# Kernel optimization log

Measured on AMD Instinct MI355X. Metric: run time of the kernel, lower is better.

## Reference

```python
import jax, jax.numpy as jnp
import numpy as np
import math

DIMS = [2048, 1024, 512, 4096]
NH, DK, DV = 16, 64, 64
BS = 8192
D_MODEL = NH * DK  # 1024


def setup_inputs() -> dict:
    key = jax.random.key(0)
    ks = jax.random.split(key, 3 * len(DIMS) + 5)
    inp = {"input_data": jax.random.normal(ks[0], (BS, sum(DIMS)), jnp.float32)}
    ki = 1
    for i, d in enumerate(DIMS):
        inp[f"wq{i}"] = jax.random.normal(ks[ki], (NH * DK, d), jnp.float32) * 0.02; ki += 1
        inp[f"wk{i}"] = jax.random.normal(ks[ki], (NH * DK, d), jnp.float32) * 0.02; ki += 1
        inp[f"wv{i}"] = jax.random.normal(ks[ki], (NH * DV, d), jnp.float32) * 0.02; ki += 1
    inp["fc_w"] = jax.random.normal(ks[ki], (NH * DV, NH * DV), jnp.float32) * 0.02; ki += 1
    inp["fc_b"] = jax.random.normal(ks[ki], (NH * DV,), jnp.float32) * 0.02; ki += 1
    inp["ln_g"] = jnp.ones((NH * DV,), jnp.float32)
    inp["ln_b"] = jnp.zeros((NH * DV,), jnp.float32)
    return inp


def _forward(input_data, wqs, wks, wvs, fc_w, fc_b, ln_g, ln_b):
    bs = input_data.shape[0]
    M = len(DIMS)
    offs = np.cumsum([0] + DIMS)
    # per-modality projections; stack into [bs, M, NH*D]
    xs = [input_data[:, offs[i]:offs[i + 1]] for i in range(M)]
    q = jnp.stack([x @ w.T for x, w in zip(xs, wqs)], axis=1)  # [bs, M, NH*DK]
    k = jnp.stack([x @ w.T for x, w in zip(xs, wks)], axis=1)
    v = jnp.stack([x @ w.T for x, w in zip(xs, wvs)], axis=1)  # [bs, M, NH*DV]
    residual = v  # v.transpose(1,2).view == original stacked v
    qh = q.reshape(bs, M, NH, DK).transpose(0, 2, 1, 3)  # [bs, NH, M, DK]
    kh = k.reshape(bs, M, NH, DK).transpose(0, 2, 1, 3)
    vh = v.reshape(bs, M, NH, DV).transpose(0, 2, 1, 3)
    scores = jnp.einsum('bhqd,bhkd->bhqk', qh, kh) / math.sqrt(DK)
    attn = jax.nn.softmax(scores, axis=-1)  # [bs, NH, M, M]
    ctx = jnp.einsum('bhqk,bhkd->bhqd', attn, vh)  # [bs, NH, M, DV]
    ctx = ctx.transpose(0, 2, 1, 3).reshape(bs, M, NH * DV)
    out = ctx @ fc_w.T + fc_b  # dropout is identity (p=0 / eval)
    out = out + residual
    mu = jnp.mean(out, axis=-1, keepdims=True)
    var = jnp.var(out, axis=-1, keepdims=True)
    out = (out - mu) / jnp.sqrt(var + 1e-6) * ln_g + ln_b
    return out, attn


def reference(input_data, wq0, wk0, wv0, wq1, wk1, wv1, wq2, wk2, wv2,
              wq3, wk3, wv3, fc_w, fc_b, ln_g, ln_b):
    wqs = [wq0, wq1, wq2, wq3]
    wks = [wk0, wk1, wk2, wk3]
    wvs = [wv0, wv1, wv2, wv3]
    return _forward(input_data, wqs, wks, wvs, fc_w, fc_b, ln_g, ln_b)
```

## Files before the change

### kernel.cpp

```cpp
#include <hip/hip_runtime.h>


typedef unsigned short u16;
typedef short short8 __attribute__((ext_vector_type(8)));
typedef float f32x4 __attribute__((ext_vector_type(4)));

__device__ __forceinline__ u16 f2bf(float f) {
  unsigned u = __builtin_bit_cast(unsigned, f);
  u += 0x7FFFu + ((u >> 16) & 1u);
  return (u16)(u >> 16);
}
__device__ __forceinline__ float bf2f(u16 s) {
  return __builtin_bit_cast(float, ((unsigned)s) << 16);
}

__device__ __forceinline__ void gload16(const u16* g, u16* l) {
  __builtin_amdgcn_global_load_lds(
      (const __attribute__((address_space(1))) void*)g,
      (__attribute__((address_space(3))) void*)l, 16, 0, 0);
}

#define CFENCE asm volatile("" ::: "memory")

struct CArgs {
  const float* src[14];
  unsigned long dst[14];
  int blk0[14];
  int n4[14];
};

__global__ __launch_bounds__(256) void convall(CArgs a, u16* __restrict__ wsb) {
  int blk = blockIdx.x;
  int s = 0;
#pragma unroll
  for (int i = 1; i < 14; ++i) s = (blk >= a.blk0[i]) ? i : s;
  int li = (blk - a.blk0[s]) * 256 + threadIdx.x;
  if (li < a.n4[s]) {
    float4 v = ((const float4*)a.src[s])[li];
    ushort4 o;
    o.x = f2bf(v.x); o.y = f2bf(v.y); o.z = f2bf(v.z); o.w = f2bf(v.w);
    ((ushort4*)(wsb + a.dst[s]))[li] = o;
  }
}

template <int MODE>
__global__ __launch_bounds__(512, 2)
void gemm8(const u16* __restrict__ Abase, int lda,
           const u16* __restrict__ Wbase, u16* __restrict__ Cq,
           u16* __restrict__ Cpre, const float* __restrict__ bias,
           const u16* __restrict__ resid) {
  __shared__ __align__(16) u16 lds[65536];

  const int tid = threadIdx.x;
  const int w = tid >> 6, lane = tid & 63;
  const int lr = lane & 15, lk = lane >> 4;
  const int wm = w >> 2, wn = w & 3;

  int K, nt, bx, by, coff;
  const u16 *A, *B;
  if (MODE == 0) {
    int seg = blockIdx.x / 384;
    int r = blockIdx.x % 384;
    bx = r % 12; by = r / 12;
    K = 4096 >> seg; nt = 128 >> seg;
    int xo, wo, mod;
    switch (seg) {
      case 0:  xo = 3584; wo = 11010048; mod = 3; break;
      case 1:  xo = 0;    wo = 0;        mod = 0; break;
      case 2:  xo = 2048; wo = 6291456;  mod = 1; break;
      default: xo = 3072; wo = 9437184;  mod = 2; break;
    }
    coff = mod * 3072;
    A = Abase + xo;
    B = Wbase + wo;
  } else {
    bx = blockIdx.x & 3; by = blockIdx.x >> 2;
    K = 1024; nt = 32; coff = 0;
    A = Abase; B = Wbase;
  }
  const size_t brow = (size_t)by * 256;
  const int bcol = bx * 256;
  const u16* Ab = A + brow * (size_t)lda;
  const u16* Bb = B + (size_t)bcol * (size_t)K;

  const int stg_k = ((lane & 3) ^ ((lane >> 3) & 3)) * 8;
  const int stg_row = lane >> 2;
  const int fso = (lk ^ ((lr >> 1) & 3)) * 8;

  f32x4 acc[8][4];
#pragma unroll
  for (int i = 0; i < 8; ++i)
#pragma unroll
    for (int j = 0; j < 4; ++j) acc[i][j] = (f32x4){0.f, 0.f, 0.f, 0.f};

  auto stageA = [&](int p) {
    const int bb = (p & 3) * 16384;
    const int k0 = p * 32;
#pragma unroll
    for (int h = 0; h < 2; ++h)
      gload16(Ab + (size_t)(h * 128 + w * 16 + stg_row) * lda + k0 + stg_k,
              (u16*)&lds[bb + h * 4096 + w * 512]);
  };
  auto stageB = [&](int p) {
    const int bb = (p & 3) * 16384 + 8192;
    const int k0 = p * 32;
#pragma unroll
    for (int h = 0; h < 2; ++h)
      gload16(Bb + (size_t)(h * 128 + w * 16 + stg_row) * (size_t)K + k0 + stg_k,
              (u16*)&lds[bb + h * 4096 + w * 512]);
  };

  stageA(0); stageB(0);
  stageA(1); stageB(1);
  stageA(2); stageB(2);
  asm volatile("s_waitcnt vmcnt(8)" ::: "memory");
  __builtin_amdgcn_s_barrier();
  CFENCE;

#pragma unroll 1
  for (int t = 0; t < nt; ++t) {
    const int bb = (t & 3) * 16384;
    short8 af[4], bfr[4];
#pragma unroll
    for (int mi = 0; mi < 4; ++mi)
      af[mi] = *(const short8*)&lds[bb + (wm * 128 + mi * 16 + lr) * 32 + fso];
#pragma unroll
    for (int ni = 0; ni < 4; ++ni)
      bfr[ni] = *(const short8*)&lds[bb + 8192 + (wn * 64 + ni * 16 + lr) * 32 + fso];
    if (t + 3 < nt) stageA(t + 3);
    CFENCE;
    __builtin_amdgcn_s_barrier();
    CFENCE;
    __builtin_amdgcn_s_setprio(1);
#pragma unroll
    for (int mi = 0; mi < 4; ++mi)
#pragma unroll
      for (int ni = 0; ni < 4; ++ni)
        acc[mi][ni] = __builtin_amdgcn_mfma_f32_16x16x32_bf16(
            af[mi], bfr[ni], acc[mi][ni], 0, 0, 0);
    __builtin_amdgcn_s_setprio(0);
    CFENCE;
    __builtin_amdgcn_s_barrier();
    CFENCE;
#pragma unroll
    for (int mi = 0; mi < 4; ++mi)
      af[mi] = *(const short8*)&lds[bb + (wm * 128 + (4 + mi) * 16 + lr) * 32 + fso];
    if (t + 3 < nt) stageB(t + 3);
    CFENCE;
    __builtin_amdgcn_s_barrier();
    CFENCE;
    __builtin_amdgcn_s_setprio(1);
#pragma unroll
    for (int mi = 0; mi < 4; ++mi)
#pragma unroll
      for (int ni = 0; ni < 4; ++ni)
        acc[mi + 4][ni] = __builtin_amdgcn_mfma_f32_16x16x32_bf16(
            af[mi], bfr[ni], acc[mi + 4][ni], 0, 0, 0);
    __builtin_amdgcn_s_setprio(0);
    CFENCE;
    if (t + 1 < nt) {
      if (t + 3 < nt)      asm volatile("s_waitcnt vmcnt(8)" ::: "memory");
      else if (t + 2 < nt) asm volatile("s_waitcnt vmcnt(4)" ::: "memory");
      else                 asm volatile("s_waitcnt vmcnt(0)" ::: "memory");
    }
    CFENCE;
    __builtin_amdgcn_s_barrier();
    CFENCE;
  }

  if (MODE == 0) {
#pragma unroll
    for (int mi = 0; mi < 8; ++mi)
#pragma unroll
      for (int ni = 0; ni < 4; ++ni) {
        const int c = coff + bcol + wn * 64 + ni * 16 + lr;
#pragma unroll
        for (int j = 0; j < 4; ++j) {
          size_t r = brow + wm * 128 + mi * 16 + lk * 4 + j;
          Cq[r * 12288 + c] = f2bf(acc[mi][ni][j]);
        }
      }
  } else {
#pragma unroll
    for (int mi = 0; mi < 8; ++mi)
#pragma unroll
      for (int ni = 0; ni < 4; ++ni) {
        const int c = bcol + wn * 64 + ni * 16 + lr;
        const float bs = bias[c];
#pragma unroll
        for (int j = 0; j < 4; ++j) {
          size_t r = brow + wm * 128 + mi * 16 + lk * 4 + j;
          size_t ridx = (r >> 2) * 12288 + (r & 3) * 3072 + 2048 + c;
          Cpre[r * 1024 + c] = f2bf(acc[mi][ni][j] + bs + bf2f(resid[ridx]));
        }
      }
  }
}

__global__ __launch_bounds__(256) void attn_k(const u16* __restrict__ qkv,
                                              u16* __restrict__ ctxb,
                                              float* __restrict__ attn_out) {
  const int tid = threadIdx.x;
  const int l = tid & 63;
  const int wg = blockIdx.x * 4 + (tid >> 6);
  const int b = wg >> 2;
  const int h0 = (wg & 3) << 2;
  const size_t base = (size_t)b * 12288 + h0 * 64 + l * 4;

  float q[4][4], k[4][4], v[4][4];
#pragma unroll
  for (int m = 0; m < 4; ++m) {
    ushort4 uq = *(const ushort4*)(qkv + base + m * 3072);
    ushort4 uk = *(const ushort4*)(qkv + base + m * 3072 + 1024);
    ushort4 uv = *(const ushort4*)(qkv + base + m * 3072 + 2048);
    q[m][0] = bf2f(uq.x); q[m][1] = bf2f(uq.y); q[m][2] = bf2f(uq.z); q[m][3] = bf2f(uq.w);
    k[m][0] = bf2f(uk.x); k[m][1] = bf2f(uk.y); k[m][2] = bf2f(uk.z); k[m][3] = bf2f(uk.w);
    v[m][0] = bf2f(uv.x); v[m][1] = bf2f(uv.y); v[m][2] = bf2f(uv.z); v[m][3] = bf2f(uv.w);
  }

  float s[16];
#pragma unroll
  for (int i = 0; i < 4; ++i)
#pragma unroll
    for (int j = 0; j < 4; ++j) {
      float acc = q[i][0] * k[j][0];
      acc += q[i][1] * k[j][1];
      acc += q[i][2] * k[j][2];
      acc += q[i][3] * k[j][3];
      s[i * 4 + j] = acc;
    }
#pragma unroll
  for (int off = 1; off < 16; off <<= 1) {
#pragma unroll
    for (int t = 0; t < 16; ++t) s[t] += __shfl_xor(s[t], off);
  }

  float a[16];
#pragma unroll
  for (int i = 0; i < 4; ++i) {
    float s0 = s[i * 4 + 0] * 0.125f, s1 = s[i * 4 + 1] * 0.125f;
    float s2 = s[i * 4 + 2] * 0.125f, s3 = s[i * 4 + 3] * 0.125f;
    float m = fmaxf(fmaxf(s0, s1), fmaxf(s2, s3));
    float e0 = __expf(s0 - m), e1 = __expf(s1 - m);
    float e2 = __expf(s2 - m), e3 = __expf(s3 - m);
    float inv = 1.0f / (e0 + e1 + e2 + e3);
    a[i * 4 + 0] = e0 * inv; a[i * 4 + 1] = e1 * inv;
    a[i * 4 + 2] = e2 * inv; a[i * 4 + 3] = e3 * inv;
  }

#pragma unroll
  for (int i = 0; i < 4; ++i) {
    float c0 = a[i*4+0]*v[0][0] + a[i*4+1]*v[1][0] + a[i*4+2]*v[2][0] + a[i*4+3]*v[3][0];
    float c1 = a[i*4+0]*v[0][1] + a[i*4+1]*v[1][1] + a[i*4+2]*v[2][1] + a[i*4+3]*v[3][1];
    float c2 = a[i*4+0]*v[0][2] + a[i*4+1]*v[1][2] + a[i*4+2]*v[2][2] + a[i*4+3]*v[3][2];
    float c3 = a[i*4+0]*v[0][3] + a[i*4+1]*v[1][3] + a[i*4+2]*v[2][3] + a[i*4+3]*v[3][3];
    ushort4 o;
    o.x = f2bf(c0); o.y = f2bf(c1); o.z = f2bf(c2); o.w = f2bf(c3);
    *(ushort4*)(ctxb + (size_t)b * 4096 + i * 1024 + h0 * 64 + l * 4) = o;
  }

  int sel = l & 15;
  float val = a[0];
#pragma unroll
  for (int t = 1; t < 16; ++t) val = (sel == t) ? a[t] : val;
  attn_out[(size_t)b * 256 + h0 * 16 + l] = val;
}

__global__ __launch_bounds__(256) void ln_k(const u16* __restrict__ pre,
                                            const float* __restrict__ g,
                                            const float* __restrict__ b,
                                            float* __restrict__ out) {
  int row = blockIdx.x;
  int tid = threadIdx.x;
  ushort4 u = *(const ushort4*)(pre + (size_t)row * 1024 + tid * 4);
  float x0 = bf2f(u.x), x1 = bf2f(u.y), x2 = bf2f(u.z), x3 = bf2f(u.w);
  float s = x0 + x1 + x2 + x3;
  float s2 = x0 * x0 + x1 * x1 + x2 * x2 + x3 * x3;
#pragma unroll
  for (int off = 32; off; off >>= 1) {
    s += __shfl_xor(s, off);
    s2 += __shfl_xor(s2, off);
  }
  __shared__ float r1[4], r2[4];
  int w = tid >> 6, lane = tid & 63;
  if (lane == 0) { r1[w] = s; r2[w] = s2; }
  __syncthreads();
  s = r1[0] + r1[1] + r1[2] + r1[3];
  s2 = r2[0] + r2[1] + r2[2] + r2[3];
  float mu = s * (1.0f / 1024.0f);
  float inv = rsqrtf(s2 * (1.0f / 1024.0f) - mu * mu + 1e-6f);
  float4 gv = *(const float4*)(g + tid * 4);
  float4 bv = *(const float4*)(b + tid * 4);
  float4 o;
  o.x = (x0 - mu) * inv * gv.x + bv.x;
  o.y = (x1 - mu) * inv * gv.y + bv.y;
  o.z = (x2 - mu) * inv * gv.z + bv.z;
  o.w = (x3 - mu) * inv * gv.w + bv.w;
  *(float4*)(out + (size_t)row * 1024 + tid * 4) = o;
}

extern "C" void kernel_launch(void* const* d_in, const int* in_sizes, int n_in,
                              void* d_out, int out_size, void* d_ws,
                              size_t ws_size, hipStream_t stream) {
  const float* fcb = (const float*)d_in[14];
  const float* lng = (const float*)d_in[15];
  const float* lnb = (const float*)d_in[16];

  u16* wsb = (u16*)d_ws;
  u16* xb = wsb;
  u16* wb = xb + 62914560;
  u16* qkv = wb + 24641536;
  u16* ctxb = qkv + 100663296;
  u16* pre = wsb;
  float* outp = (float*)d_out;
  float* attn_out = outp + 33554432;

  static const unsigned long woff[13] = {
      0,        2097152,  4194304,
      6291456,  7340032,  8388608,
      9437184,  9961472,  10485760,
      11010048, 15204352, 19398656,
      23592960};
  static const int wn4[13] = {524288, 524288, 524288, 262144, 262144, 262144,
                              131072, 131072, 131072, 1048576, 1048576, 1048576,
                              262144};

  CArgs ca;
  ca.src[0] = (const float*)d_in[0];
  ca.dst[0] = 0;
  ca.n4[0] = 62914560 / 4;
  ca.blk0[0] = 0;
  int nb = ca.n4[0] / 256;
  for (int i = 0; i < 13; ++i) {
    ca.src[i + 1] = (const float*)d_in[1 + i];
    ca.dst[i + 1] = 62914560ul + woff[i];
    ca.n4[i + 1] = wn4[i];
    ca.blk0[i + 1] = nb;
    nb += (wn4[i] + 255) / 256;
  }
  convall<<<dim3(nb), 256, 0, stream>>>(ca, wsb);

  gemm8<0><<<dim3(1536), 512, 0, stream>>>(xb, 7680, wb, qkv, nullptr, nullptr,
                                           nullptr);

  attn_k<<<dim3(8192), 256, 0, stream>>>(qkv, ctxb, attn_out);

  gemm8<1><<<dim3(512), 512, 0, stream>>>(ctxb, 1024, wb + 23592960, nullptr,
                                          pre, fcb, qkv);

  ln_k<<<dim3(32768), 256, 0, stream>>>(pre, lng, lnb, outp);
}
```

Measured before the change: 652.2 us.

## Restructure GEMM main loop to 64-wide K tiles with quadrant ping-pong schedule

Doubles the K step per iteration from 32 to 64 and replaces the 4-deep 32-wide staging ring with a double-buffered layout split into A and B halves. A new XOR swizzle over 128-byte LDS rows is meant to avoid bank conflicts. Each iteration runs four MFMA quadrants, interleaving LDS fragment loads and next-tile global-to-LDS staging between barriers. The goal is fewer loop iterations and barriers per unit of work and better overlap of memory traffic with MFMA, at the cost of a shallower prefetch depth and more complex wait-count bookkeeping.

```diff
diff --git a/kernel.cpp b/kernel.cpp
--- a/kernel.cpp
+++ b/kernel.cpp
@@ -62,7 +62,7 @@
     int seg = blockIdx.x / 384;
     int r = blockIdx.x % 384;
     bx = r % 12; by = r / 12;
-    K = 4096 >> seg; nt = 128 >> seg;
+    K = 4096 >> seg; nt = 64 >> seg;
     int xo, wo, mod;
     switch (seg) {
       case 0:  xo = 3584; wo = 11010048; mod = 3; break;
@@ -75,7 +75,7 @@
     B = Wbase + wo;
   } else {
     bx = blockIdx.x & 3; by = blockIdx.x >> 2;
-    K = 1024; nt = 32; coff = 0;
+    K = 1024; nt = 16; coff = 0;
     A = Abase; B = Wbase;
   }
   const size_t brow = (size_t)by * 256;
@@ -83,89 +83,136 @@
   const u16* Ab = A + brow * (size_t)lda;
   const u16* Bb = B + (size_t)bcol * (size_t)K;
 
-  const int stg_k = ((lane & 3) ^ ((lane >> 3) & 3)) * 8;
-  const int stg_row = lane >> 2;
-  const int fso = (lk ^ ((lr >> 1) & 3)) * 8;
-
   f32x4 acc[8][4];
 #pragma unroll
   for (int i = 0; i < 8; ++i)
 #pragma unroll
     for (int j = 0; j < 4; ++j) acc[i][j] = (f32x4){0.f, 0.f, 0.f, 0.f};
 
-  auto stageA = [&](int p) {
-    const int bb = (p & 3) * 16384;
-    const int k0 = p * 32;
-#pragma unroll
-    for (int h = 0; h < 2; ++h)
-      gload16(Ab + (size_t)(h * 128 + w * 16 + stg_row) * lda + k0 + stg_k,
-              (u16*)&lds[bb + h * 4096 + w * 512]);
-  };
-  auto stageB = [&](int p) {
-    const int bb = (p & 3) * 16384 + 8192;
-    const int k0 = p * 32;
-#pragma unroll
-    for (int h = 0; h < 2; ++h)
-      gload16(Bb + (size_t)(h * 128 + w * 16 + stg_row) * (size_t)K + k0 + stg_k,
-              (u16*)&lds[bb + h * 4096 + w * 512]);
-  };
-
-  stageA(0); stageB(0);
-  stageA(1); stageB(1);
-  stageA(2); stageB(2);
-  asm volatile("s_waitcnt vmcnt(8)" ::: "memory");
+  auto stageA = [&](int p, int half) {
+    const int base = (p & 1) * 65536 + half * 16384;
+    const int k0 = p * 64;
+#pragma unroll
+    for (int l = 0; l < 2; ++l) {
+      int s = l * 8192 + tid * 16;
+      int rw = s >> 7;
+      int ck = ((s >> 4) & 7) ^ (rw & 7);
+      int row = (rw & 63) + ((rw >> 6) << 7) + half * 64;
+      gload16(Ab + (size_t)row * lda + k0 + ck * 8, &lds[(base + s) >> 1]);
+    }
+  };
+  auto stageB = [&](int p, int half) {
+    const int base = (p & 1) * 65536 + 32768 + half * 16384;
+    const int k0 = p * 64;
+#pragma unroll
+    for (int l = 0; l < 2; ++l) {
+      int s = l * 8192 + tid * 16;
+      int rw = s >> 7;
+      int ck = ((s >> 4) & 7) ^ (rw & 7);
+      int col = (rw & 31) + ((rw >> 5) << 6) + half * 32;
+      gload16(Bb + (size_t)col * (size_t)K + k0 + ck * 8, &lds[(base + s) >> 1]);
+    }
+  };
+
+  auto ldA = [&](int t, int half, short8* dst) {
+    const u16* lp = lds + (((t & 1) * 65536 + half * 16384) >> 1);
+#pragma unroll
+    for (int mi = 0; mi < 4; ++mi) {
+      int rw = mi * 16 + lr + wm * 64;
+#pragma unroll
+      for (int ks = 0; ks < 2; ++ks) {
+        int pc = (ks * 4 + lk) ^ (rw & 7);
+        dst[mi * 2 + ks] = *(const short8*)(lp + rw * 64 + pc * 8);
+      }
+    }
+  };
+  auto ldB = [&](int t, int half, short8* dst) {
+    const u16* lp = lds + (((t & 1) * 65536 + 32768 + half * 16384) >> 1);
+#pragma unroll
+    for (int ni = 0; ni < 2; ++ni) {
+      int rw = ni * 16 + lr + wn * 32;
+#pragma unroll
+      for (int ks = 0; ks < 2; ++ks) {
+        int pc = (ks * 4 + lk) ^ (rw & 7);
+        dst[ni * 2 + ks] = *(const short8*)(lp + rw * 64 + pc * 8);
+      }
+    }
+  };
+
+  short8 af[8], bl[4], bh[4];
+  auto MQ = [&](short8* a, short8* b, int mo, int no) {
+#pragma unroll
+    for (int mi = 0; mi < 4; ++mi)
+#pragma unroll
+      for (int ni = 0; ni < 2; ++ni) {
+        acc[mo + mi][no + ni] = __builtin_amdgcn_mfma_f32_16x16x32_bf16(
+            a[mi * 2 + 0], b[ni * 2 + 0], acc[mo + mi][no + ni], 0, 0, 0);
+        acc[mo + mi][no + ni] = __builtin_amdgcn_mfma_f32_16x16x32_bf16(
+            a[mi * 2 + 1], b[ni * 2 + 1], acc[mo + mi][no + ni], 0, 0, 0);
+      }
+  };
+
+  stageA(0, 0); stageB(0, 0); stageB(0, 1); stageA(0, 1);
+  asm volatile("s_waitcnt vmcnt(4)" ::: "memory");
   __builtin_amdgcn_s_barrier();
   CFENCE;
 
 #pragma unroll 1
   for (int t = 0; t < nt; ++t) {
-    const int bb = (t & 3) * 16384;
-    short8 af[4], bfr[4];
-#pragma unroll
-    for (int mi = 0; mi < 4; ++mi)
-      af[mi] = *(const short8*)&lds[bb + (wm * 128 + mi * 16 + lr) * 32 + fso];
-#pragma unroll
-    for (int ni = 0; ni < 4; ++ni)
-      bfr[ni] = *(const short8*)&lds[bb + 8192 + (wn * 64 + ni * 16 + lr) * 32 + fso];
-    if (t + 3 < nt) stageA(t + 3);
-    CFENCE;
-    __builtin_amdgcn_s_barrier();
-    CFENCE;
+    const bool more = (t + 1 < nt);
+    ldA(t, 0, af);
+    ldB(t, 0, bl);
+    if (more) stageA(t + 1, 0);
+    CFENCE;
+    __builtin_amdgcn_s_barrier();
+    asm volatile("s_waitcnt lgkmcnt(0)" ::: "memory");
+    __builtin_amdgcn_sched_barrier(0);
     __builtin_amdgcn_s_setprio(1);
-#pragma unroll
-    for (int mi = 0; mi < 4; ++mi)
-#pragma unroll
-      for (int ni = 0; ni < 4; ++ni)
-        acc[mi][ni] = __builtin_amdgcn_mfma_f32_16x16x32_bf16(
-            af[mi], bfr[ni], acc[mi][ni], 0, 0, 0);
+    MQ(af, bl, 0, 0);
     __builtin_amdgcn_s_setprio(0);
     CFENCE;
-    __builtin_amdgcn_s_barrier();
-    CFENCE;
-#pragma unroll
-    for (int mi = 0; mi < 4; ++mi)
-      af[mi] = *(const short8*)&lds[bb + (wm * 128 + (4 + mi) * 16 + lr) * 32 + fso];
-    if (t + 3 < nt) stageB(t + 3);
-    CFENCE;
-    __builtin_amdgcn_s_barrier();
-    CFENCE;
+    if (more) asm volatile("s_waitcnt vmcnt(4)" ::: "memory");
+    else      asm volatile("s_waitcnt vmcnt(2)" ::: "memory");
+    __builtin_amdgcn_s_barrier();
+    CFENCE;
+    ldB(t, 1, bh);
+    if (more) stageB(t + 1, 0);
+    CFENCE;
+    __builtin_amdgcn_s_barrier();
+    asm volatile("s_waitcnt lgkmcnt(0)" ::: "memory");
+    __builtin_amdgcn_sched_barrier(0);
     __builtin_amdgcn_s_setprio(1);
-#pragma unroll
-    for (int mi = 0; mi < 4; ++mi)
-#pragma unroll
-      for (int ni = 0; ni < 4; ++ni)
-        acc[mi + 4][ni] = __builtin_amdgcn_mfma_f32_16x16x32_bf16(
-            af[mi], bfr[ni], acc[mi + 4][ni], 0, 0, 0);
+    MQ(af, bh, 0, 2);
     __builtin_amdgcn_s_setprio(0);
     CFENCE;
-    if (t + 1 < nt) {
-      if (t + 3 < nt)      asm volatile("s_waitcnt vmcnt(8)" ::: "memory");
-      else if (t + 2 < nt) asm volatile("s_waitcnt vmcnt(4)" ::: "memory");
-      else                 asm volatile("s_waitcnt vmcnt(0)" ::: "memory");
-    }
-    CFENCE;
-    __builtin_amdgcn_s_barrier();
-    CFENCE;
+    if (more) asm volatile("s_waitcnt vmcnt(4)" ::: "memory");
+    else      asm volatile("s_waitcnt vmcnt(0)" ::: "memory");
+    __builtin_amdgcn_s_barrier();
+    CFENCE;
+    ldA(t, 1, af);
+    if (more) stageB(t + 1, 1);
+    CFENCE;
+    __builtin_amdgcn_s_barrier();
+    asm volatile("s_waitcnt lgkmcnt(0)" ::: "memory");
+    __builtin_amdgcn_sched_barrier(0);
+    __builtin_amdgcn_s_setprio(1);
+    MQ(af, bh, 4, 2);
+    __builtin_amdgcn_s_setprio(0);
+    CFENCE;
+    __builtin_amdgcn_s_barrier();
+    CFENCE;
+    if (more) stageA(t + 1, 1);
+    CFENCE;
+    __builtin_amdgcn_s_barrier();
+    __builtin_amdgcn_s_setprio(1);
+    MQ(af, bl, 4, 0);
+    __builtin_amdgcn_s_setprio(0);
+    CFENCE;
+    if (more) {
+      asm volatile("s_waitcnt vmcnt(4)" ::: "memory");
+      __builtin_amdgcn_s_barrier();
+      CFENCE;
+    }
   }
 
   if (MODE == 0) {
```

Measured after the change: 617.0 us. 1.06x faster.
